# Optimization experiments

Measured on AMD Instinct MI355X. Metric: run time of the kernel, lower is better.

## Reference

```python
import jax, jax.numpy as jnp
import numpy as np

B, S, D, H = 256, 512, 200, 256

def setup_inputs() -> dict:
    key = jax.random.key(0)
    ks = jax.random.split(key, 10)
    scale = 1.0 / np.sqrt(D + H)
    all_input = jax.random.normal(ks[0], (B, S, D), dtype=jnp.float32)
    # realistic variable-length mask: first L tokens valid per example
    lengths = jax.random.randint(ks[1], (B,), S // 4, S + 1)
    mask = (jnp.arange(S)[None, :] < lengths[:, None]).astype(jnp.float32)
    def W(k):
        return jax.random.normal(k, (D + H, H), dtype=jnp.float32) * scale
    return {
        "all_input": all_input,
        "mask": mask,
        "Wi": W(ks[2]), "bi": jnp.zeros((H,), jnp.float32),
        "Wf": W(ks[3]), "bf": jnp.zeros((H,), jnp.float32),
        "Wo": W(ks[4]), "bo": jnp.zeros((H,), jnp.float32),
        "Wz": W(ks[5]), "bz": jnp.zeros((H,), jnp.float32),
    }

def reference(all_input, mask, Wi, bi, Wf, bf, Wo, bo, Wz, bz):
    # manually unrolled LSTM (4 gate Linears over concat(x, h)), zero init state
    def step(carry, xt):
        h, c = carry
        xh = jnp.concatenate([xt, h], axis=1)          # [B, D+H]
        i = jax.nn.sigmoid(xh @ Wi + bi)
        f = jax.nn.sigmoid(xh @ Wf + bf)
        o = jax.nn.sigmoid(xh @ Wo + bo)
        z = jnp.tanh(xh @ Wz + bz)
        c_new = i * z + f * c
        h_new = o * jnp.tanh(c_new)
        return (h_new, c_new), h_new

    h0 = jnp.zeros((all_input.shape[0], Wi.shape[1]), all_input.dtype)
    c0 = jnp.zeros_like(h0)
    xs = jnp.swapaxes(all_input, 0, 1)                  # [S, B, D]
    _, h_all = jax.lax.scan(step, (h0, c0), xs)         # [S, B, H]
    h_all = jnp.swapaxes(h_all, 0, 1)                   # [B, S, H]
    masked_h = h_all * mask[:, :, None]
    # return_average=True: masked mean over time
    return jnp.sum(masked_h, axis=1) / jnp.sum(mask, axis=1, keepdims=True)
```

## Files before the change

### kernel.cpp

```cpp
#include <hip/hip_runtime.h>
#include <hip/hip_fp16.h>

#define B_ 256
#define S_ 512
#define D_ 200
#define H_ 256

typedef _Float16 half2_t __attribute__((ext_vector_type(2)));
typedef _Float16 half8_t __attribute__((ext_vector_type(8)));
typedef float    floatx4 __attribute__((ext_vector_type(4)));

__device__ __forceinline__ float fast_sig(float x) {
    return 1.f / (1.f + __expf(-x));
}
__device__ __forceinline__ float fast_tanh(float x) {
    x = fminf(15.f, fmaxf(-15.f, x));
    float e = __expf(2.f * x);
    return (e - 1.f) / (e + 1.f);
}

__global__ void prep(const float* __restrict__ Wi, const float* __restrict__ Wf,
                     const float* __restrict__ Wo, const float* __restrict__ Wz,
                     _Float16* __restrict__ W4T, _Float16* __restrict__ WhT) {
    const int n = blockIdx.x;
    const int t = threadIdx.x;
    const int g = n >> 8, j = n & 255;
    const float* Wg = (g == 0) ? Wi : (g == 1) ? Wf : (g == 2) ? Wo : Wz;
    if (t < 224)
        W4T[(size_t)n * 224 + t] = (t < D_) ? (_Float16)Wg[t * 256 + j] : (_Float16)0.f;
    WhT[(size_t)n * 256 + t] = (_Float16)Wg[(D_ + t) * 256 + j];
}

__global__ __launch_bounds__(256) void gemm_x(const float* __restrict__ X,
                                              const _Float16* __restrict__ W4T,
                                              const float* __restrict__ bi,
                                              const float* __restrict__ bfg,
                                              const float* __restrict__ bo,
                                              const float* __restrict__ bz,
                                              _Float16* __restrict__ G2) {
    __shared__ __align__(16) _Float16 As[128][40];
    __shared__ __align__(16) _Float16 Bs[128][40];

    const int mt = blockIdx.x >> 3;
    const int nt = blockIdx.x & 7;
    const int m0 = mt * 128, n0 = nt * 128;
    const int tid  = threadIdx.x;
    const int lane = tid & 63, wave = tid >> 6;
    const int quad = lane >> 4, l16 = lane & 15;
    const int mq = (wave & 1) * 64, nq = (wave >> 1) * 64;

    floatx4 acc[4][4];
#pragma unroll
    for (int i = 0; i < 4; ++i)
#pragma unroll
        for (int j = 0; j < 4; ++j) acc[i][j] = (floatx4){0.f, 0.f, 0.f, 0.f};

    const int srow = tid >> 1;
    const int koff = (tid & 1) * 16;

    for (int kt = 0; kt < 7; ++kt) {
        const int k0 = kt * 32;
        {
            const int m = m0 + srow;
            const float* xr = X + (size_t)m * D_ + (k0 + koff);
            half8_t v0, v1;
            if (m < B_ * S_ - 1) {
                const floatx4* xp = (const floatx4*)xr;
                floatx4 f0 = xp[0], f1 = xp[1], f2 = xp[2], f3 = xp[3];
#pragma unroll
                for (int i = 0; i < 4; ++i) {
                    v0[i]     = (_Float16)f0[i];
                    v0[4 + i] = (_Float16)f1[i];
                    v1[i]     = (_Float16)f2[i];
                    v1[4 + i] = (_Float16)f3[i];
                }
            } else {
#pragma unroll
                for (int i = 0; i < 8; ++i) {
                    int k = k0 + koff + i;
                    v0[i] = (k < D_) ? (_Float16)xr[i] : (_Float16)0.f;
                }
#pragma unroll
                for (int i = 0; i < 8; ++i) {
                    int k = k0 + koff + 8 + i;
                    v1[i] = (k < D_) ? (_Float16)xr[8 + i] : (_Float16)0.f;
                }
            }
            *(half8_t*)&As[srow][koff]     = v0;
            *(half8_t*)&As[srow][koff + 8] = v1;
        }
        {
            const _Float16* wr = W4T + (size_t)(n0 + srow) * 224 + (k0 + koff);
            const half8_t* wp = (const half8_t*)wr;
            *(half8_t*)&Bs[srow][koff]     = wp[0];
            *(half8_t*)&Bs[srow][koff + 8] = wp[1];
        }
        __syncthreads();

        half8_t af[4], bf[4];
#pragma unroll
        for (int i = 0; i < 4; ++i) af[i] = *(const half8_t*)&As[mq + i * 16 + l16][quad * 8];
#pragma unroll
        for (int i = 0; i < 4; ++i) bf[i] = *(const half8_t*)&Bs[nq + i * 16 + l16][quad * 8];
#pragma unroll
        for (int mi = 0; mi < 4; ++mi)
#pragma unroll
            for (int ni = 0; ni < 4; ++ni)
                acc[mi][ni] = __builtin_amdgcn_mfma_f32_16x16x32_f16(af[mi], bf[ni], acc[mi][ni], 0, 0, 0);
        __syncthreads();
    }

    const int bb = m0 >> 9;
    const int sbase0 = (m0 & 511) + mq + quad * 4;
#pragma unroll
    for (int ni = 0; ni < 4; ++ni) {
        const int gcol = n0 + nq + ni * 16 + l16;
        const int g = gcol >> 8, j = gcol & 255;
        const int jb = j >> 4, wv = jb >> 1, jbh = jb & 1;
        const int mi2 = jbh * 4 + g, q2 = (j >> 2) & 3, r2 = j & 3;
        const float bv = ((g == 0) ? bi : (g == 1) ? bfg : (g == 2) ? bo : bz)[j];
        const size_t base = ((((size_t)bb * 8 + wv) * 4 + q2) * 512 + sbase0) * 32
                            + (size_t)mi2 * 4 + r2;
#pragma unroll
        for (int mi = 0; mi < 4; ++mi)
#pragma unroll
            for (int r = 0; r < 4; ++r)
                G2[base + (size_t)(mi * 16 + r) * 32] = (_Float16)(acc[mi][ni][r] + bv);
    }
}

__global__ __launch_bounds__(512, 2) void lstm_rec(
    const _Float16* __restrict__ G2,
    const _Float16* __restrict__ WhT,
    const float* __restrict__ mask,
    float* __restrict__ out)
{
    __shared__ __align__(16) half8_t  WLfrag[8192];
    __shared__ __align__(16) _Float16 hS[2][256];

    const int b    = blockIdx.x;
    const int t    = threadIdx.x;
    const int w    = t >> 6;
    const int lane = t & 63;
    const int l16  = lane & 15, quad = lane >> 4;

#pragma unroll
    for (int mi = 0; mi < 8; ++mi) {
        const int gcol = ((mi & 3) << 8) + (2 * w + (mi >> 2)) * 16 + l16;
        const half8_t* src = (const half8_t*)(WhT + (size_t)gcol * 256);
        WLfrag[((w * 8 + mi) * 2 + 0) * 64 + lane] = src[6 * 4 + quad];
        WLfrag[((w * 8 + mi) * 2 + 1) * 64 + lane] = src[7 * 4 + quad];
    }

#define DECLF(mi) half8_t F##mi##_0, F##mi##_1, F##mi##_2, F##mi##_3, F##mi##_4, F##mi##_5
#define LOADF(mi) do {                                                        \
        const int gcol = ((mi & 3) << 8) + (2 * w + ((mi) >> 2)) * 16 + l16;  \
        const half8_t* p = (const half8_t*)(WhT + (size_t)gcol * 256);        \
        F##mi##_0 = p[0 * 4 + quad]; F##mi##_1 = p[1 * 4 + quad];             \
        F##mi##_2 = p[2 * 4 + quad]; F##mi##_3 = p[3 * 4 + quad];             \
        F##mi##_4 = p[4 * 4 + quad]; F##mi##_5 = p[5 * 4 + quad];             \
        asm volatile("" : "+v"(F##mi##_0), "+v"(F##mi##_1), "+v"(F##mi##_2),  \
                          "+v"(F##mi##_3), "+v"(F##mi##_4), "+v"(F##mi##_5)); \
    } while (0)
    DECLF(0); DECLF(1); DECLF(2); DECLF(3); DECLF(4); DECLF(5); DECLF(6); DECLF(7);
    LOADF(0); LOADF(1); LOADF(2); LOADF(3); LOADF(4); LOADF(5); LOADF(6); LOADF(7);

    const half8_t* Gp = (const half8_t*)(G2 + (((size_t)b * 8 + w) * 4 + quad) * 512 * 32);

    if (t < 256) hS[0][t] = (_Float16)0.f;

    const int jbh_c = (l16 >> 2) & 1;
    const int r_c   = l16 & 3;
    const int j     = 32 * w + jbh_c * 16 + quad * 4 + r_c;

    float cst = 0.f, accum = 0.f, msum = 0.f;
    const float* mb = mask + (size_t)b * S_;

    half8_t G0 = Gp[0], G1 = Gp[1], G2c = Gp[2], G3 = Gp[3];

    __syncthreads();

#define MFALL(kt, Bv)                                                          \
    C0 = __builtin_amdgcn_mfma_f32_16x16x32_f16(F0_##kt, Bv, C0, 0, 0, 0);     \
    C1 = __builtin_amdgcn_mfma_f32_16x16x32_f16(F1_##kt, Bv, C1, 0, 0, 0);     \
    C2 = __builtin_amdgcn_mfma_f32_16x16x32_f16(F2_##kt, Bv, C2, 0, 0, 0);     \
    C3 = __builtin_amdgcn_mfma_f32_16x16x32_f16(F3_##kt, Bv, C3, 0, 0, 0);     \
    C4 = __builtin_amdgcn_mfma_f32_16x16x32_f16(F4_##kt, Bv, C4, 0, 0, 0);     \
    C5 = __builtin_amdgcn_mfma_f32_16x16x32_f16(F5_##kt, Bv, C5, 0, 0, 0);     \
    C6 = __builtin_amdgcn_mfma_f32_16x16x32_f16(F6_##kt, Bv, C6, 0, 0, 0);     \
    C7 = __builtin_amdgcn_mfma_f32_16x16x32_f16(F7_##kt, Bv, C7, 0, 0, 0)

#define MFLDS(ktL, Bv)                                                         \
    C0 = __builtin_amdgcn_mfma_f32_16x16x32_f16(WLfrag[((w*8+0)*2+(ktL))*64+lane], Bv, C0, 0, 0, 0); \
    C1 = __builtin_amdgcn_mfma_f32_16x16x32_f16(WLfrag[((w*8+1)*2+(ktL))*64+lane], Bv, C1, 0, 0, 0); \
    C2 = __builtin_amdgcn_mfma_f32_16x16x32_f16(WLfrag[((w*8+2)*2+(ktL))*64+lane], Bv, C2, 0, 0, 0); \
    C3 = __builtin_amdgcn_mfma_f32_16x16x32_f16(WLfrag[((w*8+3)*2+(ktL))*64+lane], Bv, C3, 0, 0, 0); \
    C4 = __builtin_amdgcn_mfma_f32_16x16x32_f16(WLfrag[((w*8+4)*2+(ktL))*64+lane], Bv, C4, 0, 0, 0); \
    C5 = __builtin_amdgcn_mfma_f32_16x16x32_f16(WLfrag[((w*8+5)*2+(ktL))*64+lane], Bv, C5, 0, 0, 0); \
    C6 = __builtin_amdgcn_mfma_f32_16x16x32_f16(WLfrag[((w*8+6)*2+(ktL))*64+lane], Bv, C6, 0, 0, 0); \
    C7 = __builtin_amdgcn_mfma_f32_16x16x32_f16(WLfrag[((w*8+7)*2+(ktL))*64+lane], Bv, C7, 0, 0, 0)

    for (int s = 0; s < S_; ++s) {
        const float m = mb[s];
        const _Float16* hb = hS[s & 1];

        floatx4 C0, C1, C2, C3, C4, C5, C6, C7;
#pragma unroll
        for (int k = 0; k < 4; ++k) {
            C0[k] = (float)G0[k];  C1[k] = (float)G0[4 + k];
            C2[k] = (float)G1[k];  C3[k] = (float)G1[4 + k];
            C4[k] = (float)G2c[k]; C5[k] = (float)G2c[4 + k];
            C6[k] = (float)G3[k];  C7[k] = (float)G3[4 + k];
        }
        const int sn = (s < S_ - 1) ? s + 1 : s;

        half8_t Bv;
        Bv = *(const half8_t*)(hb + 0 * 32 + quad * 8);  MFALL(0, Bv);
        G0 = Gp[(size_t)sn * 4 + 0]; G1 = Gp[(size_t)sn * 4 + 1];
        Bv = *(const half8_t*)(hb + 1 * 32 + quad * 8);  MFALL(1, Bv);
        Bv = *(const half8_t*)(hb + 2 * 32 + quad * 8);  MFALL(2, Bv);
        Bv = *(const half8_t*)(hb + 3 * 32 + quad * 8);  MFALL(3, Bv);
        G2c = Gp[(size_t)sn * 4 + 2]; G3 = Gp[(size_t)sn * 4 + 3];
        Bv = *(const half8_t*)(hb + 4 * 32 + quad * 8);  MFALL(4, Bv);
        Bv = *(const half8_t*)(hb + 5 * 32 + quad * 8);  MFALL(5, Bv);
        Bv = *(const half8_t*)(hb + 6 * 32 + quad * 8);  MFLDS(0, Bv);
        Bv = *(const half8_t*)(hb + 7 * 32 + quad * 8);  MFLDS(1, Bv);

        floatx4 s0 = jbh_c ? C4 : C0;
        floatx4 s1 = jbh_c ? C5 : C1;
        floatx4 s2 = jbh_c ? C6 : C2;
        floatx4 s3 = jbh_c ? C7 : C3;
        float pre[4];
        {
            floatx4 cg = s0;
            float v01 = (r_c & 1) ? cg[1] : cg[0], v23 = (r_c & 1) ? cg[3] : cg[2];
            pre[0] = (r_c & 2) ? v23 : v01;
            cg = s1; v01 = (r_c & 1) ? cg[1] : cg[0]; v23 = (r_c & 1) ? cg[3] : cg[2];
            pre[1] = (r_c & 2) ? v23 : v01;
            cg = s2; v01 = (r_c & 1) ? cg[1] : cg[0]; v23 = (r_c & 1) ? cg[3] : cg[2];
            pre[2] = (r_c & 2) ? v23 : v01;
            cg = s3; v01 = (r_c & 1) ? cg[1] : cg[0]; v23 = (r_c & 1) ? cg[3] : cg[2];
            pre[3] = (r_c & 2) ? v23 : v01;
        }
        const float fi = fast_sig(pre[0]);
        const float ff = fast_sig(pre[1]);
        const float fo = fast_sig(pre[2]);
        const float fz = fast_tanh(pre[3]);
        cst = fi * fz + ff * cst;
        const float h = fo * fast_tanh(cst);
        accum += m * h;
        msum  += m;
        if (l16 < 8) hS[(s + 1) & 1][j] = (_Float16)h;
        __syncthreads();
    }
#undef MFALL
#undef MFLDS
#undef DECLF
#undef LOADF

    if (l16 < 8) out[b * 256 + j] = accum / msum;
}

extern "C" void kernel_launch(void* const* d_in, const int* in_sizes, int n_in,
                              void* d_out, int out_size, void* d_ws, size_t ws_size,
                              hipStream_t stream) {
    const float* X    = (const float*)d_in[0];
    const float* mask = (const float*)d_in[1];
    const float* Wi   = (const float*)d_in[2];
    const float* bi   = (const float*)d_in[3];
    const float* Wf   = (const float*)d_in[4];
    const float* bf   = (const float*)d_in[5];
    const float* Wo   = (const float*)d_in[6];
    const float* bo   = (const float*)d_in[7];
    const float* Wz   = (const float*)d_in[8];
    const float* bz   = (const float*)d_in[9];
    float* out = (float*)d_out;

    char* ws = (char*)d_ws;
    _Float16* G2  = (_Float16*)ws;
    _Float16* W4T = (_Float16*)(ws + (size_t)B_ * S_ * 1024 * 2);
    _Float16* WhT = (_Float16*)(ws + (size_t)B_ * S_ * 1024 * 2 + (size_t)1024 * 224 * 2);

    hipLaunchKernelGGL(prep,     dim3(1024), dim3(256), 0, stream, Wi, Wf, Wo, Wz, W4T, WhT);
    hipLaunchKernelGGL(gemm_x,   dim3(8192), dim3(256), 0, stream, X, W4T, bi, bf, bo, bz, G2);
    hipLaunchKernelGGL(lstm_rec, dim3(B_),   dim3(512), 0, stream, G2, WhT, mask, out);
}
```

Before: 1.511 ms.

## Store gate preactivations row-major and reorder recurrent LDS loads and MFMAs

The x-projection GEMM now writes gate preactivations in plain row-major [B*S, 1024] layout instead of a permuted layout matched to the recurrence fragments. The recurrent kernel reads them as eight 4-half loads per step rather than four 8-half loads. The h-vector LDS reads are hoisted ahead of the MFMA chain, and the LDS-sourced weight MFMAs are moved earlier so their latency can overlap the register-sourced ones. The GEMM epilogue may store with better coalescing, but the recurrence now does more, narrower, strided global loads per step.

```diff
diff --git a/kernel.cpp b/kernel.cpp
--- a/kernel.cpp
+++ b/kernel.cpp
@@ -7,6 +7,7 @@
 #define H_ 256
 
 typedef _Float16 half2_t __attribute__((ext_vector_type(2)));
+typedef _Float16 half4_t __attribute__((ext_vector_type(4)));
 typedef _Float16 half8_t __attribute__((ext_vector_type(8)));
 typedef float    floatx4 __attribute__((ext_vector_type(4)));
 
@@ -37,7 +38,7 @@
                                               const float* __restrict__ bfg,
                                               const float* __restrict__ bo,
                                               const float* __restrict__ bz,
-                                              _Float16* __restrict__ G2) {
+                                              _Float16* __restrict__ G) {
     __shared__ __align__(16) _Float16 As[128][40];
     __shared__ __align__(16) _Float16 Bs[128][40];
 
@@ -110,27 +111,23 @@
         __syncthreads();
     }
 
-    const int bb = m0 >> 9;
-    const int sbase0 = (m0 & 511) + mq + quad * 4;
 #pragma unroll
     for (int ni = 0; ni < 4; ++ni) {
         const int gcol = n0 + nq + ni * 16 + l16;
         const int g = gcol >> 8, j = gcol & 255;
-        const int jb = j >> 4, wv = jb >> 1, jbh = jb & 1;
-        const int mi2 = jbh * 4 + g, q2 = (j >> 2) & 3, r2 = j & 3;
         const float bv = ((g == 0) ? bi : (g == 1) ? bfg : (g == 2) ? bo : bz)[j];
-        const size_t base = ((((size_t)bb * 8 + wv) * 4 + q2) * 512 + sbase0) * 32
-                            + (size_t)mi2 * 4 + r2;
 #pragma unroll
         for (int mi = 0; mi < 4; ++mi)
 #pragma unroll
-            for (int r = 0; r < 4; ++r)
-                G2[base + (size_t)(mi * 16 + r) * 32] = (_Float16)(acc[mi][ni][r] + bv);
+            for (int r = 0; r < 4; ++r) {
+                const int grow = m0 + mq + mi * 16 + quad * 4 + r;
+                G[(size_t)grow * 1024 + gcol] = (_Float16)(acc[mi][ni][r] + bv);
+            }
     }
 }
 
 __global__ __launch_bounds__(512, 2) void lstm_rec(
-    const _Float16* __restrict__ G2,
+    const _Float16* __restrict__ G,
     const _Float16* __restrict__ WhT,
     const float* __restrict__ mask,
     float* __restrict__ out)
@@ -165,8 +162,6 @@
     DECLF(0); DECLF(1); DECLF(2); DECLF(3); DECLF(4); DECLF(5); DECLF(6); DECLF(7);
     LOADF(0); LOADF(1); LOADF(2); LOADF(3); LOADF(4); LOADF(5); LOADF(6); LOADF(7);
 
-    const half8_t* Gp = (const half8_t*)(G2 + (((size_t)b * 8 + w) * 4 + quad) * 512 * 32);
-
     if (t < 256) hS[0][t] = (_Float16)0.f;
 
     const int jbh_c = (l16 >> 2) & 1;
@@ -176,8 +171,18 @@
     float cst = 0.f, accum = 0.f, msum = 0.f;
     const float* mb = mask + (size_t)b * S_;
 
-    half8_t G0 = Gp[0], G1 = Gp[1], G2c = Gp[2], G3 = Gp[3];
-
+    const _Float16* Gbase = G + ((size_t)b << 19) + 32 * w + quad * 4;
+
+    half4_t N0, N1, N2, N3, N4, N5, N6, N7;
+#define GLOAD(sidx) do {                                                      \
+        const _Float16* gp = Gbase + ((size_t)(sidx) << 10);                  \
+        N0 = *(const half4_t*)(gp + 0);   N1 = *(const half4_t*)(gp + 256);   \
+        N2 = *(const half4_t*)(gp + 512); N3 = *(const half4_t*)(gp + 768);   \
+        N4 = *(const half4_t*)(gp + 16);  N5 = *(const half4_t*)(gp + 272);   \
+        N6 = *(const half4_t*)(gp + 528); N7 = *(const half4_t*)(gp + 784);   \
+    } while (0)
+
+    GLOAD(0);
     __syncthreads();
 
 #define MFALL(kt, Bv)                                                          \
@@ -204,48 +209,53 @@
         const float m = mb[s];
         const _Float16* hb = hS[s & 1];
 
+        half8_t Bv0 = *(const half8_t*)(hb + 0 * 32 + quad * 8);
+        half8_t Bv1 = *(const half8_t*)(hb + 1 * 32 + quad * 8);
+        half8_t Bv2 = *(const half8_t*)(hb + 2 * 32 + quad * 8);
+        half8_t Bv3 = *(const half8_t*)(hb + 3 * 32 + quad * 8);
+
         floatx4 C0, C1, C2, C3, C4, C5, C6, C7;
 #pragma unroll
         for (int k = 0; k < 4; ++k) {
-            C0[k] = (float)G0[k];  C1[k] = (float)G0[4 + k];
-            C2[k] = (float)G1[k];  C3[k] = (float)G1[4 + k];
-            C4[k] = (float)G2c[k]; C5[k] = (float)G2c[4 + k];
-            C6[k] = (float)G3[k];  C7[k] = (float)G3[4 + k];
-        }
-        const int sn = (s < S_ - 1) ? s + 1 : s;
-
-        half8_t Bv;
-        Bv = *(const half8_t*)(hb + 0 * 32 + quad * 8);  MFALL(0, Bv);
-        G0 = Gp[(size_t)sn * 4 + 0]; G1 = Gp[(size_t)sn * 4 + 1];
-        Bv = *(const half8_t*)(hb + 1 * 32 + quad * 8);  MFALL(1, Bv);
-        Bv = *(const half8_t*)(hb + 2 * 32 + quad * 8);  MFALL(2, Bv);
-        Bv = *(const half8_t*)(hb + 3 * 32 + quad * 8);  MFALL(3, Bv);
-        G2c = Gp[(size_t)sn * 4 + 2]; G3 = Gp[(size_t)sn * 4 + 3];
-        Bv = *(const half8_t*)(hb + 4 * 32 + quad * 8);  MFALL(4, Bv);
-        Bv = *(const half8_t*)(hb + 5 * 32 + quad * 8);  MFALL(5, Bv);
-        Bv = *(const half8_t*)(hb + 6 * 32 + quad * 8);  MFLDS(0, Bv);
-        Bv = *(const half8_t*)(hb + 7 * 32 + quad * 8);  MFLDS(1, Bv);
+            C0[k] = (float)N0[k]; C1[k] = (float)N1[k];
+            C2[k] = (float)N2[k]; C3[k] = (float)N3[k];
+            C4[k] = (float)N4[k]; C5[k] = (float)N5[k];
+            C6[k] = (float)N6[k]; C7[k] = (float)N7[k];
+        }
+        GLOAD((s < S_ - 1) ? s + 1 : s);
+
+        MFALL(0, Bv0);
+        half8_t Bv4 = *(const half8_t*)(hb + 4 * 32 + quad * 8);
+        half8_t Bv5 = *(const half8_t*)(hb + 5 * 32 + quad * 8);
+        MFALL(1, Bv1);
+        half8_t Bv6 = *(const half8_t*)(hb + 6 * 32 + quad * 8);
+        half8_t Bv7 = *(const half8_t*)(hb + 7 * 32 + quad * 8);
+        MFALL(2, Bv2);
+        MFALL(3, Bv3);
+        MFLDS(0, Bv6);
+        MFLDS(1, Bv7);
+        MFALL(4, Bv4);
+        MFALL(5, Bv5);
 
         floatx4 s0 = jbh_c ? C4 : C0;
         floatx4 s1 = jbh_c ? C5 : C1;
         floatx4 s2 = jbh_c ? C6 : C2;
         floatx4 s3 = jbh_c ? C7 : C3;
-        float pre[4];
+        float pre0, pre1, pre2, pre3;
         {
-            floatx4 cg = s0;
-            float v01 = (r_c & 1) ? cg[1] : cg[0], v23 = (r_c & 1) ? cg[3] : cg[2];
-            pre[0] = (r_c & 2) ? v23 : v01;
-            cg = s1; v01 = (r_c & 1) ? cg[1] : cg[0]; v23 = (r_c & 1) ? cg[3] : cg[2];
-            pre[1] = (r_c & 2) ? v23 : v01;
-            cg = s2; v01 = (r_c & 1) ? cg[1] : cg[0]; v23 = (r_c & 1) ? cg[3] : cg[2];
-            pre[2] = (r_c & 2) ? v23 : v01;
-            cg = s3; v01 = (r_c & 1) ? cg[1] : cg[0]; v23 = (r_c & 1) ? cg[3] : cg[2];
-            pre[3] = (r_c & 2) ? v23 : v01;
-        }
-        const float fi = fast_sig(pre[0]);
-        const float ff = fast_sig(pre[1]);
-        const float fo = fast_sig(pre[2]);
-        const float fz = fast_tanh(pre[3]);
+            float v01 = (r_c & 1) ? s0[1] : s0[0], v23 = (r_c & 1) ? s0[3] : s0[2];
+            pre0 = (r_c & 2) ? v23 : v01;
+            v01 = (r_c & 1) ? s1[1] : s1[0]; v23 = (r_c & 1) ? s1[3] : s1[2];
+            pre1 = (r_c & 2) ? v23 : v01;
+            v01 = (r_c & 1) ? s2[1] : s2[0]; v23 = (r_c & 1) ? s2[3] : s2[2];
+            pre2 = (r_c & 2) ? v23 : v01;
+            v01 = (r_c & 1) ? s3[1] : s3[0]; v23 = (r_c & 1) ? s3[3] : s3[2];
+            pre3 = (r_c & 2) ? v23 : v01;
+        }
+        const float fi = fast_sig(pre0);
+        const float ff = fast_sig(pre1);
+        const float fo = fast_sig(pre2);
+        const float fz = fast_tanh(pre3);
         cst = fi * fz + ff * cst;
         const float h = fo * fast_tanh(cst);
         accum += m * h;
@@ -257,6 +267,7 @@
 #undef MFLDS
 #undef DECLF
 #undef LOADF
+#undef GLOAD
 
     if (l16 < 8) out[b * 256 + j] = accum / msum;
 }
@@ -277,11 +288,11 @@
     float* out = (float*)d_out;
 
     char* ws = (char*)d_ws;
-    _Float16* G2  = (_Float16*)ws;
+    _Float16* G   = (_Float16*)ws;
     _Float16* W4T = (_Float16*)(ws + (size_t)B_ * S_ * 1024 * 2);
     _Float16* WhT = (_Float16*)(ws + (size_t)B_ * S_ * 1024 * 2 + (size_t)1024 * 224 * 2);
 
     hipLaunchKernelGGL(prep,     dim3(1024), dim3(256), 0, stream, Wi, Wf, Wo, Wz, W4T, WhT);
-    hipLaunchKernelGGL(gemm_x,   dim3(8192), dim3(256), 0, stream, X, W4T, bi, bf, bo, bz, G2);
-    hipLaunchKernelGGL(lstm_rec, dim3(B_),   dim3(512), 0, stream, G2, WhT, mask, out);
-}
+    hipLaunchKernelGGL(gemm_x,   dim3(8192), dim3(256), 0, stream, X, W4T, bi, bf, bo, bz, G);
+    hipLaunchKernelGGL(lstm_rec, dim3(B_),   dim3(512), 0, stream, G, WhT, mask, out);
+}
```

Result: faster. 1.278 ms (-15.4%).
